# Kernel optimization log

Measured on AMD Instinct MI355X. Metric: run time of the kernel, lower is better.

The kernel has to match this reference:

```python
import jax, jax.numpy as jnp
import numpy as np

HEADS = 8
NEG_SLOPE = 0.2
N_REL = 3
N_NODES = 10000
N_EDGES = 160000
OBS = 32
ACT = 8
N_GRAPHS = 16
HC = HEADS * OBS  # 256 = heads * out_channels (dim=1)


def _rgat_layer(x, w, q, k, e, we, b, src, dst, etype, eattr):
    """PyG RGATConv, additive-self-attention, across-relation, dim=1, concat=True, eval mode."""
    N = x.shape[0]
    # relation-specific transform for every node, then per-edge gather (avoids [E,in,out] bmm)
    xw = jnp.einsum('ni,rio->nro', x, w)              # [N, R, H*C]
    outi = xw[dst, etype]                              # [E, H*C] target features
    outj = xw[src, etype]                              # [E, H*C] source features
    alpha = outi @ q + outj @ k + (eattr @ we) @ e     # [E, H]
    alpha = jax.nn.leaky_relu(alpha, NEG_SLOPE)
    # segment softmax over destination neighborhoods (PyG softmax: detached max, +1e-16)
    amax = jax.lax.stop_gradient(jax.ops.segment_max(alpha, dst, num_segments=N))
    amax = jnp.where(jnp.isfinite(amax), amax, 0.0)
    ex = jnp.exp(alpha - amax[dst])
    denom = jax.ops.segment_sum(ex, dst, num_segments=N)
    attn = ex / (denom[dst] + 1e-16)                   # [E, H]
    E_ = outj.shape[0]
    msg = attn[:, :, None] * outj.reshape(E_, HEADS, -1)  # [E, H, C]
    agg = jax.ops.segment_sum(msg, dst, num_segments=N)   # [N, H, C]
    return agg.reshape(N, -1) + b                          # concat heads + bias


def setup_inputs() -> dict:
    key = jax.random.key(0)
    ks = jax.random.split(key, 32)
    s = 0.05
    inp = {
        'x': jax.random.normal(ks[0], (N_NODES, OBS), jnp.float32),
        'edge_index': jax.random.randint(ks[1], (2, N_EDGES), 0, N_NODES),
        'edge_type': jax.random.randint(ks[2], (N_EDGES,), 0, N_REL),
        'edge_attr': jax.random.normal(ks[3], (N_EDGES, 1), jnp.float32),
        'batch': jnp.sort(jax.random.randint(ks[4], (N_NODES,), 0, N_GRAPHS)),
    }
    ins = [OBS, HC, HC]
    i = 5
    for l, cin in enumerate(ins, start=1):
        inp[f'w{l}'] = s * jax.random.normal(ks[i + 0], (N_REL, cin, HC), jnp.float32)
        inp[f'q{l}'] = s * jax.random.normal(ks[i + 1], (HC, HEADS), jnp.float32)
        inp[f'k{l}'] = s * jax.random.normal(ks[i + 2], (HC, HEADS), jnp.float32)
        inp[f'e{l}'] = s * jax.random.normal(ks[i + 3], (HC, HEADS), jnp.float32)
        inp[f'we{l}'] = s * jax.random.normal(ks[i + 4], (1, HC), jnp.float32)
        inp[f'b{l}'] = jnp.zeros((HC,), jnp.float32)
        i += 5
    inp['wlin'] = s * jax.random.normal(ks[i], (HC, ACT), jnp.float32)
    inp['blin'] = jnp.zeros((ACT,), jnp.float32)
    return inp


def reference(x, edge_index, edge_type, edge_attr, batch,
              w1, q1, k1, e1, we1, b1,
              w2, q2, k2, e2, we2, b2,
              w3, q3, k3, e3, we3, b3,
              wlin, blin):
    src, dst = edge_index[0], edge_index[1]
    h = jax.nn.relu(_rgat_layer(x, w1, q1, k1, e1, we1, b1, src, dst, edge_type, edge_attr))
    h = jax.nn.relu(_rgat_layer(h, w2, q2, k2, e2, we2, b2, src, dst, edge_type, edge_attr))
    h = jax.nn.relu(_rgat_layer(h, w3, q3, k3, e3, we3, b3, src, dst, edge_type, edge_attr))
    h = jnp.tanh(h @ wlin + blin)                        # [N, ACT]
    sums = jax.ops.segment_sum(h, batch, num_segments=N_GRAPHS)
    cnts = jax.ops.segment_sum(jnp.ones((h.shape[0], 1), h.dtype), batch, num_segments=N_GRAPHS)
    return sums / jnp.maximum(cnts, 1.0)                 # global_mean_pool -> [G, ACT]
```

## Files before the change

kernel.cpp:

```cpp
#include <hip/hip_runtime.h>
#include <math.h>

#define HEADS 8
#define HC 256
#define NREL 3
#define NEG 0.2f
#define MAXDEG 64
#define PCHUNK 8
#define NCT 17

typedef float vfloat4 __attribute__((ext_vector_type(4)));
typedef short b16x8 __attribute__((ext_vector_type(8)));
typedef float f32x4 __attribute__((ext_vector_type(4)));
typedef unsigned short u16x8 __attribute__((ext_vector_type(8)));

__device__ __forceinline__ float warp32_reduce(float p) {
#pragma unroll
    for (int off = 16; off > 0; off >>= 1) p += __shfl_down(p, off, 32);
    return p;
}

__device__ __forceinline__ unsigned short f2bf(float f) {
    unsigned u = __float_as_uint(f);
    unsigned r = (u + 0x7FFFu + ((u >> 16) & 1u)) >> 16;
    return (unsigned short)r;
}
__device__ __forceinline__ float bf2f(unsigned short b) {
    return __uint_as_float(((unsigned)b) << 16);
}

__global__ void k_wprep(
    const float* __restrict__ W1, const float* __restrict__ Q1, const float* __restrict__ K1,
    const float* __restrict__ E1, const float* __restrict__ WE1,
    const float* __restrict__ W2, const float* __restrict__ Q2, const float* __restrict__ K2,
    const float* __restrict__ E2, const float* __restrict__ WE2,
    const float* __restrict__ W3, const float* __restrict__ Q3, const float* __restrict__ K3,
    const float* __restrict__ E3, const float* __restrict__ WE3,
    unsigned short* __restrict__ b1hi, unsigned short* __restrict__ b1lo,
    unsigned short* __restrict__ b2hi, unsigned short* __restrict__ b2lo,
    unsigned short* __restrict__ b3hi, unsigned short* __restrict__ b3lo,
    float* __restrict__ wee,
    const float* __restrict__ x, unsigned short* __restrict__ x1hi,
    unsigned short* __restrict__ x1lo,
    const int* __restrict__ ei, const int* __restrict__ et, const float* __restrict__ ea,
    int* __restrict__ fill, int2* __restrict__ bkt,
    int nnodes, int nedges, int nwcv, int nprep, int npacka) {
    int bi = blockIdx.x;
    int tid = threadIdx.x;
    if (bi < nwcv) {
        const float* w;
        unsigned short *bhi, *blo;
        int K, r, kb;
        if (bi < NREL) { w = W1; bhi = b1hi; blo = b1lo; K = 32; r = bi; kb = 0; }
        else if (bi < NREL + NREL * 8) {
            int idx = bi - NREL; w = W2; bhi = b2hi; blo = b2lo; K = HC; r = idx >> 3; kb = idx & 7;
        } else {
            int idx = bi - NREL - NREL * 8; w = W3; bhi = b3hi; blo = b3lo; K = HC; r = idx >> 3; kb = idx & 7;
        }
        int KB = K / 32;
        int ct = tid >> 4, mc = tid & 15;
        int c = ct * 16 + mc;
#pragma unroll
        for (int q = 0; q < 4; ++q) {
            u16x8 hv, lv;
#pragma unroll
            for (int j = 0; j < 8; ++j) {
                float f = w[(size_t)(r * K + kb * 32 + q * 8 + j) * HC + c];
                unsigned short h = f2bf(f);
                hv[j] = h;
                lv[j] = f2bf(f - bf2f(h));
            }
            size_t base = ((((size_t)r * NCT + ct) * KB + kb) * 64 + q * 16 + mc) * 8;
            *(u16x8*)(bhi + base) = hv;
            *(u16x8*)(blo + base) = lv;
        }
        return;
    }
    bi -= nwcv;
    if (bi >= nprep + npacka) {
        int e = (bi - nprep - npacka) * 256 + tid;
        if (e < nedges) {
            int dst = ei[nedges + e];
            int pos = atomicAdd(&fill[dst], 1);
            if (pos < MAXDEG)
                bkt[dst * MAXDEG + pos] = make_int2((ei[e] << 2) | (et[e] & 3),
                                                    __float_as_int(ea[e]));
        }
        return;
    }
    if (bi >= nprep) {
        int i = (bi - nprep) * 256 + tid;
        if (i < nnodes * 32) {
            int n = i >> 5, k = i & 31;
            float f = x[i];
            unsigned short h = f2bf(f);
            int ntile = n >> 4, m = n & 15;
            int q = (k >> 3) & 3, j = k & 7;
            size_t o = ((size_t)ntile * 64 + q * 16 + m) * 8 + j;
            x1hi[o] = h;
            x1lo[o] = f2bf(f - bf2f(h));
        }
        return;
    }
    {
        int w = tid >> 5, lane = tid & 31;
        int row = bi * 8 + w;
        const float *wmat, *qm, *km, *em, *wem;
        unsigned short *bhi, *blo;
        int K, layer, lbi;
        if (row < NREL * 32) {
            layer = 0; lbi = row; K = 32;
            wmat = W1; qm = Q1; km = K1; em = E1; wem = WE1; bhi = b1hi; blo = b1lo;
        } else if (row < NREL * 32 + NREL * HC) {
            layer = 1; lbi = row - NREL * 32; K = HC;
            wmat = W2; qm = Q2; km = K2; em = E2; wem = WE2; bhi = b2hi; blo = b2lo;
        } else {
            layer = 2; lbi = row - NREL * 32 - NREL * HC; K = HC;
            wmat = W3; qm = Q3; km = K3; em = E3; wem = WE3; bhi = b3hi; blo = b3lo;
        }
        int r = lbi / K, i = lbi - r * K;
        int KB = K / 32;
        int kb = i >> 5, qq = (i >> 3) & 3, j = i & 7;
        const float* wrow = wmat + (size_t)lbi * HC;
        float pq[8] = {0.f, 0.f, 0.f, 0.f, 0.f, 0.f, 0.f, 0.f};
        float pk[8] = {0.f, 0.f, 0.f, 0.f, 0.f, 0.f, 0.f, 0.f};
#pragma unroll
        for (int it = 0; it < HC; it += 32) {
            int o = it + lane;
            float wv = wrow[o];
            float4 qa = *(const float4*)(qm + (size_t)o * 8);
            float4 qb = *(const float4*)(qm + (size_t)o * 8 + 4);
            float4 ka = *(const float4*)(km + (size_t)o * 8);
            float4 kc = *(const float4*)(km + (size_t)o * 8 + 4);
            pq[0] += wv * qa.x; pq[1] += wv * qa.y; pq[2] += wv * qa.z; pq[3] += wv * qa.w;
            pq[4] += wv * qb.x; pq[5] += wv * qb.y; pq[6] += wv * qb.z; pq[7] += wv * qb.w;
            pk[0] += wv * ka.x; pk[1] += wv * ka.y; pk[2] += wv * ka.z; pk[3] += wv * ka.w;
            pk[4] += wv * kc.x; pk[5] += wv * kc.y; pk[6] += wv * kc.z; pk[7] += wv * kc.w;
        }
#pragma unroll
        for (int off = 16; off > 0; off >>= 1) {
#pragma unroll
            for (int u = 0; u < 8; ++u) {
                pq[u] += __shfl_xor(pq[u], off, 32);
                pk[u] += __shfl_xor(pk[u], off, 32);
            }
        }
        size_t base = (((size_t)r * NCT + 16) * KB + kb) * 512 + j;
        if (lane < 16) {
            int h = lane & 7;
            bool isq = lane < 8;
            float v;
            switch (h) {
                case 0: v = isq ? pq[0] : pk[0]; break;
                case 1: v = isq ? pq[1] : pk[1]; break;
                case 2: v = isq ? pq[2] : pk[2]; break;
                case 3: v = isq ? pq[3] : pk[3]; break;
                case 4: v = isq ? pq[4] : pk[4]; break;
                case 5: v = isq ? pq[5] : pk[5]; break;
                case 6: v = isq ? pq[6] : pk[6]; break;
                default: v = isq ? pq[7] : pk[7]; break;
            }
            size_t o = base + (size_t)(qq * 16 + (isq ? 0 : 8) + h) * 8;
            unsigned short hh = f2bf(v);
            bhi[o] = hh;
            blo[o] = f2bf(v - bf2f(hh));
        }
        if (lbi == 0 && w == 0 && lane < HEADS) {
            float s = 0.f;
            for (int o = 0; o < HC; o++) s += wem[o] * em[o * HEADS + lane];
            wee[layer * HEADS + lane] = s;
        }
        return;
    }
}

template <int K, int NT>
__global__ __launch_bounds__(256) void k_mfma(const unsigned short* __restrict__ pahi,
                                              const unsigned short* __restrict__ palo,
                                              const unsigned short* __restrict__ pbhi,
                                              const unsigned short* __restrict__ pblo,
                                              float* __restrict__ xw,
                                              float* __restrict__ qdot,
                                              float* __restrict__ kdot,
                                              int nnodes, int ntiles) {
    constexpr int KB = K / 32;
    int ntg = blockIdx.x;
    int r = blockIdx.y;
    int t = threadIdx.x;
    int wv = t >> 6, lane = t & 63;
    int q = lane >> 4, m = lane & 15;
    f32x4 acc[5][NT] = {};
    for (int kb = 0; kb < KB; ++kb) {
        b16x8 ah[NT], al[NT];
#pragma unroll
        for (int ti = 0; ti < NT; ++ti) {
            int nt = ntg * NT + ti;
            if (nt >= ntiles) nt = ntiles - 1;
            size_t ao = (((size_t)nt * KB + kb) * 64 + lane) * 8;
            ah[ti] = *(const b16x8*)(pahi + ao);
            al[ti] = *(const b16x8*)(palo + ao);
        }
#pragma unroll
        for (int s = 0; s < 5; ++s) {
            int ct = wv + 4 * s;
            if (ct >= NCT) continue;
            size_t o = (((size_t)r * NCT + ct) * KB + kb) * 512 + (size_t)lane * 8;
            b16x8 vbh = *(const b16x8*)(pbhi + o);
            b16x8 vbl = *(const b16x8*)(pblo + o);
#pragma unroll
            for (int ti = 0; ti < NT; ++ti) {
                acc[s][ti] = __builtin_amdgcn_mfma_f32_16x16x32_bf16(ah[ti], vbh, acc[s][ti], 0, 0, 0);
                acc[s][ti] = __builtin_amdgcn_mfma_f32_16x16x32_bf16(al[ti], vbh, acc[s][ti], 0, 0, 0);
                acc[s][ti] = __builtin_amdgcn_mfma_f32_16x16x32_bf16(ah[ti], vbl, acc[s][ti], 0, 0, 0);
            }
        }
    }
#pragma unroll
    for (int ti = 0; ti < NT; ++ti) {
        int nt = ntg * NT + ti;
        if (nt >= ntiles) continue;
        int n0 = nt * 16;
#pragma unroll
        for (int s = 0; s < 5; ++s) {
            int ct = wv + 4 * s;
            if (ct >= NCT) continue;
            if (ct < 16) {
                int c = ct * 16 + m;
#pragma unroll
                for (int g = 0; g < 4; ++g) {
                    int n = n0 + q * 4 + g;
                    if (n < nnodes) xw[((size_t)n * NREL + r) * HC + c] = acc[s][ti][g];
                }
            } else {
#pragma unroll
                for (int g = 0; g < 4; ++g) {
                    int n = n0 + q * 4 + g;
                    if (n < nnodes) {
                        if (m < 8) qdot[n * 24 + r * 8 + m] = acc[s][ti][g];
                        else       kdot[n * 24 + r * 8 + (m - 8)] = acc[s][ti][g];
                    }
                }
            }
        }
    }
}

__global__ __launch_bounds__(256) void k_agg(const float* __restrict__ xw,
                      const float* __restrict__ qdot, const float* __restrict__ kdot,
                      const int* __restrict__ fill, const int2* __restrict__ bkt,
                      const float* __restrict__ wee,
                      const float* __restrict__ bias, float* __restrict__ hout,
                      unsigned short* __restrict__ houthi, unsigned short* __restrict__ houtlo,
                      int nnodes) {
    __shared__ float salpha[4][MAXDEG * HEADS];
    __shared__ int spack[4][MAXDEG];
    int wv = threadIdx.x >> 6, lane = threadIdx.x & 63;
    int n = blockIdx.x * 4 + wv;
    if (n >= nnodes) return;
    int beg = n * MAXDEG;
    int deg = fill[n];
    if (deg > MAXDEG) deg = MAXDEG;
    float* sal = salpha[wv];
    int* spk = spack[wv];
    {
        int h = lane & 7;
        float weeh = wee[h];
        const float* qdn = qdot + n * 24;
        for (int base = 0; base < deg; base += 8) {
            int d = base + (lane >> 3);
            if (d < deg) {
                int2 pa = bkt[beg + d];
                int pk = pa.x;
                float ae = __int_as_float(pa.y);
                int s = pk >> 2, t = pk & 3;
                if (h == 0) spk[d] = pk;
                float a = qdn[t * 8 + h] + kdot[s * 24 + t * 8 + h] + ae * weeh;
                sal[d * 8 + h] = (a > 0.f) ? a : NEG * a;
            }
        }
    }
    float sinv_h;
    {
        int h = lane & 7, c = lane >> 3;
        float m = -INFINITY;
        for (int d = c; d < deg; d += 8) m = fmaxf(m, sal[d * 8 + h]);
        m = fmaxf(m, __shfl_xor(m, 8, 64));
        m = fmaxf(m, __shfl_xor(m, 16, 64));
        m = fmaxf(m, __shfl_xor(m, 32, 64));
        float s = 0.f;
        for (int d = c; d < deg; d += 8) {
            float ex = expf(sal[d * 8 + h] - m);
            sal[d * 8 + h] = ex;
            s += ex;
        }
        s += __shfl_xor(s, 8, 64);
        s += __shfl_xor(s, 16, 64);
        s += __shfl_xor(s, 32, 64);
        sinv_h = 1.f / (s + 1e-16f);
    }
    float sinv_sel = __shfl(sinv_h, lane >> 3, 64);
    int hsel = lane >> 3;
    float4 acc4 = make_float4(0.f, 0.f, 0.f, 0.f);
    int d = 0;
    for (; d + 7 < deg; d += 8) {
        const float4* rp[8];
        float av[8];
#pragma unroll
        for (int u = 0; u < 8; ++u) {
            int pk = spk[d + u];
            rp[u] = (const float4*)(xw + ((size_t)(pk >> 2) * NREL + (pk & 3)) * HC);
            av[u] = sal[(d + u) * 8 + hsel];
        }
        float4 vv[8];
#pragma unroll
        for (int u = 0; u < 8; ++u) vv[u] = rp[u][lane];
#pragma unroll
        for (int u = 0; u < 8; ++u) {
            acc4.x += av[u] * vv[u].x;
            acc4.y += av[u] * vv[u].y;
            acc4.z += av[u] * vv[u].z;
            acc4.w += av[u] * vv[u].w;
        }
    }
    for (; d + 3 < deg; d += 4) {
        int pk0 = spk[d], pk1 = spk[d + 1], pk2 = spk[d + 2], pk3 = spk[d + 3];
        const float4* r0 = (const float4*)(xw + ((size_t)(pk0 >> 2) * NREL + (pk0 & 3)) * HC);
        const float4* r1 = (const float4*)(xw + ((size_t)(pk1 >> 2) * NREL + (pk1 & 3)) * HC);
        const float4* r2 = (const float4*)(xw + ((size_t)(pk2 >> 2) * NREL + (pk2 & 3)) * HC);
        const float4* r3 = (const float4*)(xw + ((size_t)(pk3 >> 2) * NREL + (pk3 & 3)) * HC);
        float4 v0 = r0[lane], v1 = r1[lane], v2 = r2[lane], v3 = r3[lane];
        float a0 = sal[d * 8 + hsel];
        float a1 = sal[(d + 1) * 8 + hsel];
        float a2 = sal[(d + 2) * 8 + hsel];
        float a3 = sal[(d + 3) * 8 + hsel];
        acc4.x += a0 * v0.x + a1 * v1.x + a2 * v2.x + a3 * v3.x;
        acc4.y += a0 * v0.y + a1 * v1.y + a2 * v2.y + a3 * v3.y;
        acc4.z += a0 * v0.z + a1 * v1.z + a2 * v2.z + a3 * v3.z;
        acc4.w += a0 * v0.w + a1 * v1.w + a2 * v2.w + a3 * v3.w;
    }
    for (; d < deg; ++d) {
        int pk = spk[d];
        const float4* r0 = (const float4*)(xw + ((size_t)(pk >> 2) * NREL + (pk & 3)) * HC);
        float4 v0 = r0[lane];
        float a0 = sal[d * 8 + hsel];
        acc4.x += a0 * v0.x;
        acc4.y += a0 * v0.y;
        acc4.z += a0 * v0.z;
        acc4.w += a0 * v0.w;
    }
    float4 bv = *(const float4*)(bias + lane * 4);
    float4 v;
    v.x = fmaxf(acc4.x * sinv_sel + bv.x, 0.f);
    v.y = fmaxf(acc4.y * sinv_sel + bv.y, 0.f);
    v.z = fmaxf(acc4.z * sinv_sel + bv.z, 0.f);
    v.w = fmaxf(acc4.w * sinv_sel + bv.w, 0.f);
    if (hout) *(float4*)(hout + (size_t)n * HC + lane * 4) = v;
    if (houthi) {
        int ntile = n >> 4, mm = n & 15;
        float vv[4] = {v.x, v.y, v.z, v.w};
#pragma unroll
        for (int i = 0; i < 4; ++i) {
            int c = lane * 4 + i;
            int kb = c >> 5, q = (c >> 3) & 3, j = c & 7;
            size_t o2 = ((((size_t)ntile * 8 + kb) * 64) + q * 16 + mm) * 8 + j;
            unsigned short hh = f2bf(vv[i]);
            houthi[o2] = hh;
            houtlo[o2] = f2bf(vv[i] - bf2f(hh));
        }
    }
}

__global__ __launch_bounds__(256) void k_pool2(const float* __restrict__ h3,
                                               const float* __restrict__ wlin,
                                               const float* __restrict__ blin,
                                               const int* __restrict__ batch,
                                               float* __restrict__ partials,
                                               int* __restrict__ gcnt, int* __restrict__ ctr,
                                               float* __restrict__ out, int nnodes, int ngraph) {
    int g = blockIdx.x / PCHUNK, chunk = blockIdx.x % PCHUNK;
    __shared__ int sb[2];
    if (threadIdx.x < 2) {
        int target = g + threadIdx.x;
        int lo = 0, hi = nnodes;
        while (lo < hi) { int mid = (lo + hi) >> 1; if (batch[mid] < target) lo = mid + 1; else hi = mid; }
        sb[threadIdx.x] = lo;
    }
    __syncthreads();
    int beg = sb[0], end = sb[1];
    int t = threadIdx.x;
    int w = t >> 6, lane = t & 63;
    int h = lane & 7, grp = lane >> 3;
    float rw[32];
#pragma unroll
    for (int k = 0; k < 8; ++k)
#pragma unroll
        for (int j = 0; j < 4; ++j)
            rw[k * 4 + j] = wlin[(grp * 4 + j + 32 * k) * HEADS + h];
    float bl = blin[h];
    float acc = 0.f;
    int wg = chunk * 4 + w;
    for (int n = beg + wg; n < end; n += PCHUNK * 4) {
        const float* row = h3 + (size_t)n * HC;
        float dot = 0.f;
#pragma unroll
        for (int k = 0; k < 8; ++k) {
            float4 v = *(const float4*)&row[grp * 4 + 32 * k];
            dot += v.x * rw[k * 4] + v.y * rw[k * 4 + 1] + v.z * rw[k * 4 + 2] + v.w * rw[k * 4 + 3];
        }
        dot += __shfl_xor(dot, 8, 64);
        dot += __shfl_xor(dot, 16, 64);
        dot += __shfl_xor(dot, 32, 64);
        acc += tanhf(dot + bl);
    }
    __shared__ float sacc[4][HEADS];
    __shared__ float sred[HEADS];
    __shared__ int slast;
    if (lane < HEADS) sacc[w][h] = acc;
    __syncthreads();
    if (t < HEADS) sred[t] = sacc[0][t] + sacc[1][t] + sacc[2][t] + sacc[3][t];
    __syncthreads();
    if (t == 0) {
        for (int hh = 0; hh < HEADS; ++hh)
            partials[(size_t)blockIdx.x * HEADS + hh] = sred[hh];
        if (chunk == 0) gcnt[g] = end - beg;
        __threadfence();
        slast = (atomicAdd(ctr, 1) == (int)gridDim.x - 1);
    }
    __syncthreads();
    if (slast) {
        __threadfence();
        if (t < ngraph * HEADS) {
            int gg = t >> 3, hh = t & 7;
            float s = 0.f;
            for (int c = 0; c < PCHUNK; ++c)
                s += partials[(size_t)(gg * PCHUNK + c) * HEADS + hh];
            out[t] = s / fmaxf((float)gcnt[gg], 1.f);
        }
    }
}


extern "C" void kernel_launch(void* const* d_in, const int* in_sizes, int n_in,
                              void* d_out, int out_size, void* d_ws, size_t ws_size,
                              hipStream_t stream) {
    const float* x    = (const float*)d_in[0];
    const int*   ei   = (const int*)d_in[1];
    const int*   et   = (const int*)d_in[2];
    const float* ea   = (const float*)d_in[3];
    const int*   batch = (const int*)d_in[4];
    const float* W[3]  = {(const float*)d_in[5],  (const float*)d_in[11], (const float*)d_in[17]};
    const float* Q[3]  = {(const float*)d_in[6],  (const float*)d_in[12], (const float*)d_in[18]};
    const float* K[3]  = {(const float*)d_in[7],  (const float*)d_in[13], (const float*)d_in[19]};
    const float* Em[3] = {(const float*)d_in[8],  (const float*)d_in[14], (const float*)d_in[20]};
    const float* WE[3] = {(const float*)d_in[9],  (const float*)d_in[15], (const float*)d_in[21]};
    const float* B[3]  = {(const float*)d_in[10], (const float*)d_in[16], (const float*)d_in[22]};
    const float* wlin = (const float*)d_in[23];
    const float* blin = (const float*)d_in[24];

    int nnodes = in_sizes[0] / 32;
    int nedges = in_sizes[2];
    int ngraph = 16;
    int npad = (nnodes + 15) & ~15;
    int ntiles = npad / 16;

    char* ws = (char*)d_ws;
    size_t off = 0;
    auto alloc = [&](size_t bytes) -> void* {
        void* p = ws + off;
        off = (off + bytes + 255) & ~(size_t)255;
        return p;
    };
    int*   fill     = (int*)alloc((size_t)(nnodes + 64) * 4);
    int*   ctr      = fill + nnodes;
    int2*  bkt      = (int2*)alloc((size_t)nnodes * MAXDEG * 8);
    float* xw       = (float*)alloc((size_t)npad * NREL * HC * 4);
    float* qdot     = (float*)alloc((size_t)npad * NREL * HEADS * 4);
    float* kdot     = (float*)alloc((size_t)npad * NREL * HEADS * 4);
    float* ha       = (float*)alloc((size_t)nnodes * HC * 4);
    float* wee      = (float*)alloc((size_t)NREL * HEADS * 4);
    float* partials = (float*)alloc((size_t)ngraph * PCHUNK * HEADS * 4);
    int*   gcnt     = (int*)alloc((size_t)ngraph * 4);
    unsigned short* x1hi = (unsigned short*)alloc((size_t)npad * 32 * 2);
    unsigned short* x1lo = (unsigned short*)alloc((size_t)npad * 32 * 2);
    unsigned short* hahi = (unsigned short*)alloc((size_t)npad * HC * 2);
    unsigned short* halo = (unsigned short*)alloc((size_t)npad * HC * 2);
    unsigned short* hbhi = (unsigned short*)alloc((size_t)npad * HC * 2);
    unsigned short* hblo = (unsigned short*)alloc((size_t)npad * HC * 2);
    unsigned short* wt1hi = (unsigned short*)alloc((size_t)NREL * NCT * 1 * 512 * 2);
    unsigned short* wt1lo = (unsigned short*)alloc((size_t)NREL * NCT * 1 * 512 * 2);
    unsigned short* wt2hi = (unsigned short*)alloc((size_t)NREL * NCT * 8 * 512 * 2);
    unsigned short* wt2lo = (unsigned short*)alloc((size_t)NREL * NCT * 8 * 512 * 2);
    unsigned short* wt3hi = (unsigned short*)alloc((size_t)NREL * NCT * 8 * 512 * 2);
    unsigned short* wt3lo = (unsigned short*)alloc((size_t)NREL * NCT * 8 * 512 * 2);
    (void)ws_size; (void)n_in; (void)out_size;

    int nwcv = NREL * (1 + 8 + 8);
    int nprep = (NREL * 32 + 2 * NREL * HC) / 8;
    int npacka = (nnodes * 32 + 255) / 256;
    int nscat = (nedges + 255) / 256;

    hipMemsetAsync(fill, 0, (size_t)(nnodes + 64) * 4, stream);
    k_wprep<<<nwcv + nprep + npacka + nscat, 256, 0, stream>>>(
        W[0], Q[0], K[0], Em[0], WE[0],
        W[1], Q[1], K[1], Em[1], WE[1],
        W[2], Q[2], K[2], Em[2], WE[2],
        wt1hi, wt1lo, wt2hi, wt2lo, wt3hi, wt3lo, wee,
        x, x1hi, x1lo,
        ei, et, ea, fill, bkt,
        nnodes, nedges, nwcv, nprep, npacka);

    dim3 gmfma((ntiles + 1) / 2, NREL);
    int gagg = (nnodes + 3) / 4;

    k_mfma<32, 2><<<gmfma, 256, 0, stream>>>(x1hi, x1lo, wt1hi, wt1lo, xw, qdot, kdot, nnodes, ntiles);
    k_agg<<<gagg, 256, 0, stream>>>(xw, qdot, kdot, fill, bkt, wee + 0, B[0],
                                    nullptr, hahi, halo, nnodes);

    k_mfma<HC, 2><<<gmfma, 256, 0, stream>>>(hahi, halo, wt2hi, wt2lo, xw, qdot, kdot, nnodes, ntiles);
    k_agg<<<gagg, 256, 0, stream>>>(xw, qdot, kdot, fill, bkt, wee + 8, B[1],
                                    nullptr, hbhi, hblo, nnodes);

    k_mfma<HC, 2><<<gmfma, 256, 0, stream>>>(hbhi, hblo, wt3hi, wt3lo, xw, qdot, kdot, nnodes, ntiles);
    k_agg<<<gagg, 256, 0, stream>>>(xw, qdot, kdot, fill, bkt, wee + 16, B[2],
                                    ha, nullptr, nullptr, nnodes);

    k_pool2<<<ngraph * PCHUNK, 256, 0, stream>>>(ha, wlin, blin, batch, partials, gcnt, ctr,
                                                 (float*)d_out, nnodes, ngraph);
}
```

Before: 300.1 us.

## Fuse final linear+tanh+mean-pool into last aggregation and pack raw x inside MFMA

The last aggregation kernel now applies the final 256x8 linear layer and tanh per node, writes an 8-wide per-node output, and the last-finishing block performs the per-graph mean pool. This removes the separate pool kernel and the full 256-wide fp32 hidden-state write and re-read. The first-layer MFMA kernel also converts raw fp32 x into bf16 hi/lo operands on the fly, which drops the packing stage from the prep kernel. In exchange each node's wave does extra shuffle reductions, and the final pooling runs serially in a single block.

```diff
diff --git a/kernel.cpp b/kernel.cpp
--- a/kernel.cpp
+++ b/kernel.cpp
@@ -6,19 +6,12 @@
 #define NREL 3
 #define NEG 0.2f
 #define MAXDEG 64
-#define PCHUNK 8
 #define NCT 17
 
 typedef float vfloat4 __attribute__((ext_vector_type(4)));
 typedef short b16x8 __attribute__((ext_vector_type(8)));
 typedef float f32x4 __attribute__((ext_vector_type(4)));
 typedef unsigned short u16x8 __attribute__((ext_vector_type(8)));
-
-__device__ __forceinline__ float warp32_reduce(float p) {
-#pragma unroll
-    for (int off = 16; off > 0; off >>= 1) p += __shfl_down(p, off, 32);
-    return p;
-}
 
 __device__ __forceinline__ unsigned short f2bf(float f) {
     unsigned u = __float_as_uint(f);
@@ -40,11 +33,9 @@
     unsigned short* __restrict__ b2hi, unsigned short* __restrict__ b2lo,
     unsigned short* __restrict__ b3hi, unsigned short* __restrict__ b3lo,
     float* __restrict__ wee,
-    const float* __restrict__ x, unsigned short* __restrict__ x1hi,
-    unsigned short* __restrict__ x1lo,
     const int* __restrict__ ei, const int* __restrict__ et, const float* __restrict__ ea,
     int* __restrict__ fill, int2* __restrict__ bkt,
-    int nnodes, int nedges, int nwcv, int nprep, int npacka) {
+    int nnodes, int nedges, int nwcv, int nprep) {
     int bi = blockIdx.x;
     int tid = threadIdx.x;
     if (bi < nwcv) {
@@ -77,28 +68,14 @@
         return;
     }
     bi -= nwcv;
-    if (bi >= nprep + npacka) {
-        int e = (bi - nprep - npacka) * 256 + tid;
+    if (bi >= nprep) {
+        int e = (bi - nprep) * 256 + tid;
         if (e < nedges) {
             int dst = ei[nedges + e];
             int pos = atomicAdd(&fill[dst], 1);
             if (pos < MAXDEG)
                 bkt[dst * MAXDEG + pos] = make_int2((ei[e] << 2) | (et[e] & 3),
                                                     __float_as_int(ea[e]));
-        }
-        return;
-    }
-    if (bi >= nprep) {
-        int i = (bi - nprep) * 256 + tid;
-        if (i < nnodes * 32) {
-            int n = i >> 5, k = i & 31;
-            float f = x[i];
-            unsigned short h = f2bf(f);
-            int ntile = n >> 4, m = n & 15;
-            int q = (k >> 3) & 3, j = k & 7;
-            size_t o = ((size_t)ntile * 64 + q * 16 + m) * 8 + j;
-            x1hi[o] = h;
-            x1lo[o] = f2bf(f - bf2f(h));
         }
         return;
     }
@@ -174,11 +151,12 @@
     }
 }
 
-template <int K, int NT>
+template <int K, int NT, bool RAWX>
 __global__ __launch_bounds__(256) void k_mfma(const unsigned short* __restrict__ pahi,
                                               const unsigned short* __restrict__ palo,
                                               const unsigned short* __restrict__ pbhi,
                                               const unsigned short* __restrict__ pblo,
+                                              const float* __restrict__ xraw,
                                               float* __restrict__ xw,
                                               float* __restrict__ qdot,
                                               float* __restrict__ kdot,
@@ -196,9 +174,23 @@
         for (int ti = 0; ti < NT; ++ti) {
             int nt = ntg * NT + ti;
             if (nt >= ntiles) nt = ntiles - 1;
-            size_t ao = (((size_t)nt * KB + kb) * 64 + lane) * 8;
-            ah[ti] = *(const b16x8*)(pahi + ao);
-            al[ti] = *(const b16x8*)(palo + ao);
+            if constexpr (RAWX) {
+                int row = nt * 16 + m;
+                if (row >= nnodes) row = nnodes - 1;
+                const float4* xr = (const float4*)(xraw + (size_t)row * 32 + q * 8);
+                float4 f0 = xr[0], f1 = xr[1];
+                float fv[8] = {f0.x, f0.y, f0.z, f0.w, f1.x, f1.y, f1.z, f1.w};
+#pragma unroll
+                for (int j = 0; j < 8; ++j) {
+                    unsigned short hh = f2bf(fv[j]);
+                    ah[ti][j] = (short)hh;
+                    al[ti][j] = (short)f2bf(fv[j] - bf2f(hh));
+                }
+            } else {
+                size_t ao = (((size_t)nt * KB + kb) * 64 + lane) * 8;
+                ah[ti] = *(const b16x8*)(pahi + ao);
+                al[ti] = *(const b16x8*)(palo + ao);
+            }
         }
 #pragma unroll
         for (int s = 0; s < 5; ++s) {
@@ -249,192 +241,198 @@
                       const float* __restrict__ qdot, const float* __restrict__ kdot,
                       const int* __restrict__ fill, const int2* __restrict__ bkt,
                       const float* __restrict__ wee,
-                      const float* __restrict__ bias, float* __restrict__ hout,
+                      const float* __restrict__ bias,
                       unsigned short* __restrict__ houthi, unsigned short* __restrict__ houtlo,
-                      int nnodes) {
+                      float* __restrict__ out8,
+                      const float* __restrict__ wlin, const float* __restrict__ blin,
+                      const int* __restrict__ batch,
+                      int* __restrict__ ctr, float* __restrict__ out,
+                      int nnodes, int ngraph) {
     __shared__ float salpha[4][MAXDEG * HEADS];
     __shared__ int spack[4][MAXDEG];
+    __shared__ float sout[4][8];
+    __shared__ int slast;
+    __shared__ int sbound[17];
+    __shared__ float spool[256];
     int wv = threadIdx.x >> 6, lane = threadIdx.x & 63;
     int n = blockIdx.x * 4 + wv;
-    if (n >= nnodes) return;
-    int beg = n * MAXDEG;
-    int deg = fill[n];
-    if (deg > MAXDEG) deg = MAXDEG;
-    float* sal = salpha[wv];
-    int* spk = spack[wv];
-    {
-        int h = lane & 7;
-        float weeh = wee[h];
-        const float* qdn = qdot + n * 24;
-        for (int base = 0; base < deg; base += 8) {
-            int d = base + (lane >> 3);
-            if (d < deg) {
-                int2 pa = bkt[beg + d];
-                int pk = pa.x;
-                float ae = __int_as_float(pa.y);
-                int s = pk >> 2, t = pk & 3;
-                if (h == 0) spk[d] = pk;
-                float a = qdn[t * 8 + h] + kdot[s * 24 + t * 8 + h] + ae * weeh;
-                sal[d * 8 + h] = (a > 0.f) ? a : NEG * a;
-            }
-        }
-    }
-    float sinv_h;
-    {
-        int h = lane & 7, c = lane >> 3;
-        float m = -INFINITY;
-        for (int d = c; d < deg; d += 8) m = fmaxf(m, sal[d * 8 + h]);
-        m = fmaxf(m, __shfl_xor(m, 8, 64));
-        m = fmaxf(m, __shfl_xor(m, 16, 64));
-        m = fmaxf(m, __shfl_xor(m, 32, 64));
-        float s = 0.f;
-        for (int d = c; d < deg; d += 8) {
-            float ex = expf(sal[d * 8 + h] - m);
-            sal[d * 8 + h] = ex;
-            s += ex;
-        }
-        s += __shfl_xor(s, 8, 64);
-        s += __shfl_xor(s, 16, 64);
-        s += __shfl_xor(s, 32, 64);
-        sinv_h = 1.f / (s + 1e-16f);
-    }
-    float sinv_sel = __shfl(sinv_h, lane >> 3, 64);
-    int hsel = lane >> 3;
-    float4 acc4 = make_float4(0.f, 0.f, 0.f, 0.f);
-    int d = 0;
-    for (; d + 7 < deg; d += 8) {
-        const float4* rp[8];
-        float av[8];
-#pragma unroll
-        for (int u = 0; u < 8; ++u) {
-            int pk = spk[d + u];
-            rp[u] = (const float4*)(xw + ((size_t)(pk >> 2) * NREL + (pk & 3)) * HC);
-            av[u] = sal[(d + u) * 8 + hsel];
-        }
-        float4 vv[8];
-#pragma unroll
-        for (int u = 0; u < 8; ++u) vv[u] = rp[u][lane];
-#pragma unroll
-        for (int u = 0; u < 8; ++u) {
-            acc4.x += av[u] * vv[u].x;
-            acc4.y += av[u] * vv[u].y;
-            acc4.z += av[u] * vv[u].z;
-            acc4.w += av[u] * vv[u].w;
-        }
-    }
-    for (; d + 3 < deg; d += 4) {
-        int pk0 = spk[d], pk1 = spk[d + 1], pk2 = spk[d + 2], pk3 = spk[d + 3];
-        const float4* r0 = (const float4*)(xw + ((size_t)(pk0 >> 2) * NREL + (pk0 & 3)) * HC);
-        const float4* r1 = (const float4*)(xw + ((size_t)(pk1 >> 2) * NREL + (pk1 & 3)) * HC);
-        const float4* r2 = (const float4*)(xw + ((size_t)(pk2 >> 2) * NREL + (pk2 & 3)) * HC);
-        const float4* r3 = (const float4*)(xw + ((size_t)(pk3 >> 2) * NREL + (pk3 & 3)) * HC);
-        float4 v0 = r0[lane], v1 = r1[lane], v2 = r2[lane], v3 = r3[lane];
-        float a0 = sal[d * 8 + hsel];
-        float a1 = sal[(d + 1) * 8 + hsel];
-        float a2 = sal[(d + 2) * 8 + hsel];
-        float a3 = sal[(d + 3) * 8 + hsel];
-        acc4.x += a0 * v0.x + a1 * v1.x + a2 * v2.x + a3 * v3.x;
-        acc4.y += a0 * v0.y + a1 * v1.y + a2 * v2.y + a3 * v3.y;
-        acc4.z += a0 * v0.z + a1 * v1.z + a2 * v2.z + a3 * v3.z;
-        acc4.w += a0 * v0.w + a1 * v1.w + a2 * v2.w + a3 * v3.w;
-    }
-    for (; d < deg; ++d) {
-        int pk = spk[d];
-        const float4* r0 = (const float4*)(xw + ((size_t)(pk >> 2) * NREL + (pk & 3)) * HC);
-        float4 v0 = r0[lane];
-        float a0 = sal[d * 8 + hsel];
-        acc4.x += a0 * v0.x;
-        acc4.y += a0 * v0.y;
-        acc4.z += a0 * v0.z;
-        acc4.w += a0 * v0.w;
-    }
-    float4 bv = *(const float4*)(bias + lane * 4);
-    float4 v;
-    v.x = fmaxf(acc4.x * sinv_sel + bv.x, 0.f);
-    v.y = fmaxf(acc4.y * sinv_sel + bv.y, 0.f);
-    v.z = fmaxf(acc4.z * sinv_sel + bv.z, 0.f);
-    v.w = fmaxf(acc4.w * sinv_sel + bv.w, 0.f);
-    if (hout) *(float4*)(hout + (size_t)n * HC + lane * 4) = v;
-    if (houthi) {
-        int ntile = n >> 4, mm = n & 15;
-        float vv[4] = {v.x, v.y, v.z, v.w};
-#pragma unroll
-        for (int i = 0; i < 4; ++i) {
-            int c = lane * 4 + i;
-            int kb = c >> 5, q = (c >> 3) & 3, j = c & 7;
-            size_t o2 = ((((size_t)ntile * 8 + kb) * 64) + q * 16 + mm) * 8 + j;
-            unsigned short hh = f2bf(vv[i]);
-            houthi[o2] = hh;
-            houtlo[o2] = f2bf(vv[i] - bf2f(hh));
-        }
-    }
-}
-
-__global__ __launch_bounds__(256) void k_pool2(const float* __restrict__ h3,
-                                               const float* __restrict__ wlin,
-                                               const float* __restrict__ blin,
-                                               const int* __restrict__ batch,
-                                               float* __restrict__ partials,
-                                               int* __restrict__ gcnt, int* __restrict__ ctr,
-                                               float* __restrict__ out, int nnodes, int ngraph) {
-    int g = blockIdx.x / PCHUNK, chunk = blockIdx.x % PCHUNK;
-    __shared__ int sb[2];
-    if (threadIdx.x < 2) {
-        int target = g + threadIdx.x;
-        int lo = 0, hi = nnodes;
-        while (lo < hi) { int mid = (lo + hi) >> 1; if (batch[mid] < target) lo = mid + 1; else hi = mid; }
-        sb[threadIdx.x] = lo;
-    }
-    __syncthreads();
-    int beg = sb[0], end = sb[1];
-    int t = threadIdx.x;
-    int w = t >> 6, lane = t & 63;
-    int h = lane & 7, grp = lane >> 3;
-    float rw[32];
-#pragma unroll
-    for (int k = 0; k < 8; ++k)
-#pragma unroll
-        for (int j = 0; j < 4; ++j)
-            rw[k * 4 + j] = wlin[(grp * 4 + j + 32 * k) * HEADS + h];
-    float bl = blin[h];
-    float acc = 0.f;
-    int wg = chunk * 4 + w;
-    for (int n = beg + wg; n < end; n += PCHUNK * 4) {
-        const float* row = h3 + (size_t)n * HC;
-        float dot = 0.f;
-#pragma unroll
-        for (int k = 0; k < 8; ++k) {
-            float4 v = *(const float4*)&row[grp * 4 + 32 * k];
-            dot += v.x * rw[k * 4] + v.y * rw[k * 4 + 1] + v.z * rw[k * 4 + 2] + v.w * rw[k * 4 + 3];
-        }
-        dot += __shfl_xor(dot, 8, 64);
-        dot += __shfl_xor(dot, 16, 64);
-        dot += __shfl_xor(dot, 32, 64);
-        acc += tanhf(dot + bl);
-    }
-    __shared__ float sacc[4][HEADS];
-    __shared__ float sred[HEADS];
-    __shared__ int slast;
-    if (lane < HEADS) sacc[w][h] = acc;
-    __syncthreads();
-    if (t < HEADS) sred[t] = sacc[0][t] + sacc[1][t] + sacc[2][t] + sacc[3][t];
-    __syncthreads();
-    if (t == 0) {
-        for (int hh = 0; hh < HEADS; ++hh)
-            partials[(size_t)blockIdx.x * HEADS + hh] = sred[hh];
-        if (chunk == 0) gcnt[g] = end - beg;
-        __threadfence();
-        slast = (atomicAdd(ctr, 1) == (int)gridDim.x - 1);
-    }
-    __syncthreads();
-    if (slast) {
-        __threadfence();
-        if (t < ngraph * HEADS) {
-            int gg = t >> 3, hh = t & 7;
+    if (n < nnodes) {
+        int beg = n * MAXDEG;
+        int deg = fill[n];
+        if (deg > MAXDEG) deg = MAXDEG;
+        float* sal = salpha[wv];
+        int* spk = spack[wv];
+        {
+            int h = lane & 7;
+            float weeh = wee[h];
+            const float* qdn = qdot + n * 24;
+            for (int base = 0; base < deg; base += 8) {
+                int d = base + (lane >> 3);
+                if (d < deg) {
+                    int2 pa = bkt[beg + d];
+                    int pk = pa.x;
+                    float ae = __int_as_float(pa.y);
+                    int s = pk >> 2, t = pk & 3;
+                    if (h == 0) spk[d] = pk;
+                    float a = qdn[t * 8 + h] + kdot[s * 24 + t * 8 + h] + ae * weeh;
+                    sal[d * 8 + h] = (a > 0.f) ? a : NEG * a;
+                }
+            }
+        }
+        float sinv_h;
+        {
+            int h = lane & 7, c = lane >> 3;
+            float m = -INFINITY;
+            for (int d = c; d < deg; d += 8) m = fmaxf(m, sal[d * 8 + h]);
+            m = fmaxf(m, __shfl_xor(m, 8, 64));
+            m = fmaxf(m, __shfl_xor(m, 16, 64));
+            m = fmaxf(m, __shfl_xor(m, 32, 64));
             float s = 0.f;
-            for (int c = 0; c < PCHUNK; ++c)
-                s += partials[(size_t)(gg * PCHUNK + c) * HEADS + hh];
-            out[t] = s / fmaxf((float)gcnt[gg], 1.f);
+            for (int d = c; d < deg; d += 8) {
+                float ex = expf(sal[d * 8 + h] - m);
+                sal[d * 8 + h] = ex;
+                s += ex;
+            }
+            s += __shfl_xor(s, 8, 64);
+            s += __shfl_xor(s, 16, 64);
+            s += __shfl_xor(s, 32, 64);
+            sinv_h = 1.f / (s + 1e-16f);
+        }
+        float sinv_sel = __shfl(sinv_h, lane >> 3, 64);
+        int hsel = lane >> 3;
+        float4 acc4 = make_float4(0.f, 0.f, 0.f, 0.f);
+        int d = 0;
+        for (; d + 7 < deg; d += 8) {
+            const float4* rp[8];
+            float av[8];
+#pragma unroll
+            for (int u = 0; u < 8; ++u) {
+                int pk = spk[d + u];
+                rp[u] = (const float4*)(xw + ((size_t)(pk >> 2) * NREL + (pk & 3)) * HC);
+                av[u] = sal[(d + u) * 8 + hsel];
+            }
+            float4 vv[8];
+#pragma unroll
+            for (int u = 0; u < 8; ++u) vv[u] = rp[u][lane];
+#pragma unroll
+            for (int u = 0; u < 8; ++u) {
+                acc4.x += av[u] * vv[u].x;
+                acc4.y += av[u] * vv[u].y;
+                acc4.z += av[u] * vv[u].z;
+                acc4.w += av[u] * vv[u].w;
+            }
+        }
+        for (; d + 3 < deg; d += 4) {
+            int pk0 = spk[d], pk1 = spk[d + 1], pk2 = spk[d + 2], pk3 = spk[d + 3];
+            const float4* r0 = (const float4*)(xw + ((size_t)(pk0 >> 2) * NREL + (pk0 & 3)) * HC);
+            const float4* r1 = (const float4*)(xw + ((size_t)(pk1 >> 2) * NREL + (pk1 & 3)) * HC);
+            const float4* r2 = (const float4*)(xw + ((size_t)(pk2 >> 2) * NREL + (pk2 & 3)) * HC);
+            const float4* r3 = (const float4*)(xw + ((size_t)(pk3 >> 2) * NREL + (pk3 & 3)) * HC);
+            float4 v0 = r0[lane], v1 = r1[lane], v2 = r2[lane], v3 = r3[lane];
+            float a0 = sal[d * 8 + hsel];
+            float a1 = sal[(d + 1) * 8 + hsel];
+            float a2 = sal[(d + 2) * 8 + hsel];
+            float a3 = sal[(d + 3) * 8 + hsel];
+            acc4.x += a0 * v0.x + a1 * v1.x + a2 * v2.x + a3 * v3.x;
+            acc4.y += a0 * v0.y + a1 * v1.y + a2 * v2.y + a3 * v3.y;
+            acc4.z += a0 * v0.z + a1 * v1.z + a2 * v2.z + a3 * v3.z;
+            acc4.w += a0 * v0.w + a1 * v1.w + a2 * v2.w + a3 * v3.w;
+        }
+        for (; d < deg; ++d) {
+            int pk = spk[d];
+            const float4* r0 = (const float4*)(xw + ((size_t)(pk >> 2) * NREL + (pk & 3)) * HC);
+            float4 v0 = r0[lane];
+            float a0 = sal[d * 8 + hsel];
+            acc4.x += a0 * v0.x;
+            acc4.y += a0 * v0.y;
+            acc4.z += a0 * v0.z;
+            acc4.w += a0 * v0.w;
+        }
+        float4 bv = *(const float4*)(bias + lane * 4);
+        float vv4[4];
+        vv4[0] = fmaxf(acc4.x * sinv_sel + bv.x, 0.f);
+        vv4[1] = fmaxf(acc4.y * sinv_sel + bv.y, 0.f);
+        vv4[2] = fmaxf(acc4.z * sinv_sel + bv.z, 0.f);
+        vv4[3] = fmaxf(acc4.w * sinv_sel + bv.w, 0.f);
+        if (houthi) {
+            int ntile = n >> 4, mm = n & 15;
+#pragma unroll
+            for (int i = 0; i < 4; ++i) {
+                int c = lane * 4 + i;
+                int kb = c >> 5, q = (c >> 3) & 3, j = c & 7;
+                size_t o2 = ((((size_t)ntile * 8 + kb) * 64) + q * 16 + mm) * 8 + j;
+                unsigned short hh = f2bf(vv4[i]);
+                houthi[o2] = hh;
+                houtlo[o2] = f2bf(vv4[i] - bf2f(hh));
+            }
+        }
+        if (out8) {
+            float part[8] = {0.f, 0.f, 0.f, 0.f, 0.f, 0.f, 0.f, 0.f};
+#pragma unroll
+            for (int i = 0; i < 4; ++i) {
+                const float4* wr = (const float4*)(wlin + (size_t)(lane * 4 + i) * 8);
+                float4 wa = wr[0], wb = wr[1];
+                float vi = vv4[i];
+                part[0] += vi * wa.x; part[1] += vi * wa.y;
+                part[2] += vi * wa.z; part[3] += vi * wa.w;
+                part[4] += vi * wb.x; part[5] += vi * wb.y;
+                part[6] += vi * wb.z; part[7] += vi * wb.w;
+            }
+#pragma unroll
+            for (int off = 32; off > 0; off >>= 1) {
+#pragma unroll
+                for (int u = 0; u < 8; ++u) part[u] += __shfl_xor(part[u], off, 64);
+            }
+            if (lane < 8) {
+                float sel;
+                switch (lane) {
+                    case 0: sel = part[0]; break;
+                    case 1: sel = part[1]; break;
+                    case 2: sel = part[2]; break;
+                    case 3: sel = part[3]; break;
+                    case 4: sel = part[4]; break;
+                    case 5: sel = part[5]; break;
+                    case 6: sel = part[6]; break;
+                    default: sel = part[7]; break;
+                }
+                sout[wv][lane] = tanhf(sel + blin[lane]);
+            }
+        }
+    }
+    if (out8) {
+        __syncthreads();
+        if (threadIdx.x == 0) {
+            int n0 = blockIdx.x * 4;
+            int nv = nnodes - n0;
+            if (nv > 4) nv = 4;
+            if (nv > 0) {
+                float4* dst4 = (float4*)(out8 + (size_t)n0 * 8);
+                const float4* s4 = (const float4*)sout;
+                for (int k = 0; k < nv * 2; ++k) dst4[k] = s4[k];
+            }
+            __threadfence();
+            slast = (atomicAdd(ctr, 1) == (int)gridDim.x - 1);
+        }
+        __syncthreads();
+        if (slast) {
+            __threadfence();
+            int t = threadIdx.x;
+            if (t < 17) {
+                int lo = 0, hi = nnodes;
+                while (lo < hi) { int mid = (lo + hi) >> 1; if (batch[mid] < t) lo = mid + 1; else hi = mid; }
+                sbound[t] = lo;
+            }
+            __syncthreads();
+            int g = t >> 4, c = (t >> 3) & 1, h = t & 7;
+            int beg = sbound[g], end = sbound[g + 1];
+            float s = 0.f;
+            for (int i = beg + c; i < end; i += 2) s += out8[(size_t)i * 8 + h];
+            spool[t] = s;
+            __syncthreads();
+            if (c == 0 && g < ngraph) {
+                float tot = spool[t] + spool[t + 8];
+                out[g * 8 + h] = tot / fmaxf((float)(end - beg), 1.f);
+            }
         }
     }
 }
@@ -476,12 +474,8 @@
     float* xw       = (float*)alloc((size_t)npad * NREL * HC * 4);
     float* qdot     = (float*)alloc((size_t)npad * NREL * HEADS * 4);
     float* kdot     = (float*)alloc((size_t)npad * NREL * HEADS * 4);
-    float* ha       = (float*)alloc((size_t)nnodes * HC * 4);
     float* wee      = (float*)alloc((size_t)NREL * HEADS * 4);
-    float* partials = (float*)alloc((size_t)ngraph * PCHUNK * HEADS * 4);
-    int*   gcnt     = (int*)alloc((size_t)ngraph * 4);
-    unsigned short* x1hi = (unsigned short*)alloc((size_t)npad * 32 * 2);
-    unsigned short* x1lo = (unsigned short*)alloc((size_t)npad * 32 * 2);
+    float* out8     = (float*)alloc((size_t)npad * 8 * 4);
     unsigned short* hahi = (unsigned short*)alloc((size_t)npad * HC * 2);
     unsigned short* halo = (unsigned short*)alloc((size_t)npad * HC * 2);
     unsigned short* hbhi = (unsigned short*)alloc((size_t)npad * HC * 2);
@@ -496,34 +490,35 @@
 
     int nwcv = NREL * (1 + 8 + 8);
     int nprep = (NREL * 32 + 2 * NREL * HC) / 8;
-    int npacka = (nnodes * 32 + 255) / 256;
     int nscat = (nedges + 255) / 256;
 
     hipMemsetAsync(fill, 0, (size_t)(nnodes + 64) * 4, stream);
-    k_wprep<<<nwcv + nprep + npacka + nscat, 256, 0, stream>>>(
+    k_wprep<<<nwcv + nprep + nscat, 256, 0, stream>>>(
         W[0], Q[0], K[0], Em[0], WE[0],
         W[1], Q[1], K[1], Em[1], WE[1],
         W[2], Q[2], K[2], Em[2], WE[2],
         wt1hi, wt1lo, wt2hi, wt2lo, wt3hi, wt3lo, wee,
-        x, x1hi, x1lo,
         ei, et, ea, fill, bkt,
-        nnodes, nedges, nwcv, nprep, npacka);
+        nnodes, nedges, nwcv, nprep);
 
     dim3 gmfma((ntiles + 1) / 2, NREL);
     int gagg = (nnodes + 3) / 4;
 
-    k_mfma<32, 2><<<gmfma, 256, 0, stream>>>(x1hi, x1lo, wt1hi, wt1lo, xw, qdot, kdot, nnodes, ntiles);
+    k_mfma<32, 2, true><<<gmfma, 256, 0, stream>>>(nullptr, nullptr, wt1hi, wt1lo, x,
+                                                   xw, qdot, kdot, nnodes, ntiles);
     k_agg<<<gagg, 256, 0, stream>>>(xw, qdot, kdot, fill, bkt, wee + 0, B[0],
-                                    nullptr, hahi, halo, nnodes);
-
-    k_mfma<HC, 2><<<gmfma, 256, 0, stream>>>(hahi, halo, wt2hi, wt2lo, xw, qdot, kdot, nnodes, ntiles);
+                                    hahi, halo, nullptr, nullptr, nullptr, nullptr,
+                                    nullptr, nullptr, nnodes, ngraph);
+
+    k_mfma<HC, 2, false><<<gmfma, 256, 0, stream>>>(hahi, halo, wt2hi, wt2lo, nullptr,
+                                                    xw, qdot, kdot, nnodes, ntiles);
     k_agg<<<gagg, 256, 0, stream>>>(xw, qdot, kdot, fill, bkt, wee + 8, B[1],
-                                    nullptr, hbhi, hblo, nnodes);
-
-    k_mfma<HC, 2><<<gmfma, 256, 0, stream>>>(hbhi, hblo, wt3hi, wt3lo, xw, qdot, kdot, nnodes, ntiles);
+                                    hbhi, hblo, nullptr, nullptr, nullptr, nullptr,
+                                    nullptr, nullptr, nnodes, ngraph);
+
+    k_mfma<HC, 2, false><<<gmfma, 256, 0, stream>>>(hbhi, hblo, wt3hi, wt3lo, nullptr,
+                                                    xw, qdot, kdot, nnodes, ntiles);
     k_agg<<<gagg, 256, 0, stream>>>(xw, qdot, kdot, fill, bkt, wee + 16, B[2],
-                                    ha, nullptr, nullptr, nnodes);
-
-    k_pool2<<<ngraph * PCHUNK, 256, 0, stream>>>(ha, wlin, blin, batch, partials, gcnt, ctr,
-                                                 (float*)d_out, nnodes, ngraph);
+                                    nullptr, nullptr, out8, wlin, blin, batch,
+                                    ctr, (float*)d_out, nnodes, ngraph);
 }
```

Result: slower. 445.1 us (+48.3%).
